# Kernel tuning notes

Measured on AMD Instinct MI355X. Metric: run time of the kernel, lower is better.

## Reference

```python
import jax, jax.numpy as jnp
import numpy as np

B, T, D, HD, HN, O = 32, 512, 512, 64, 16, 512
EPS = 1e-5


def setup_inputs() -> dict:
    key = jax.random.key(0)
    ks = jax.random.split(key, 12)
    s = lambda fan_in: 1.0 / np.sqrt(fan_in)
    inp = {
        "inputs": jax.random.normal(ks[0], (B, T, D), dtype=jnp.float32),
        "Wq": jax.random.uniform(ks[1], (HN, D, HD), jnp.float32, -s(D), s(D)),
        "bq": jnp.zeros((HN, HD), jnp.float32),
        "Wk": jax.random.uniform(ks[2], (HN, D, HD), jnp.float32, -s(D), s(D)),
        "bk": jnp.zeros((HN, HD), jnp.float32),
        "Wv": jax.random.uniform(ks[3], (HN, D, HD), jnp.float32, -s(D), s(D)),
        "bv": jnp.zeros((HN, HD), jnp.float32),
        "Wr": jax.random.uniform(ks[4], (D, O), jnp.float32, -s(D), s(D)),
        "br": jnp.zeros((O,), jnp.float32),
        "Wo": jax.random.uniform(ks[5], (HN * HD, O), jnp.float32, -s(HN * HD), s(HN * HD)),
        "bo": jnp.zeros((O,), jnp.float32),
        "ln1_w": jnp.ones((O,), jnp.float32),
        "ln1_b": jnp.zeros((O,), jnp.float32),
        "Wfc": jax.random.uniform(ks[6], (O, O), jnp.float32, -s(O), s(O)),
        "bfc": jnp.zeros((O,), jnp.float32),
        "ln2_w": jnp.ones((O,), jnp.float32),
        "ln2_b": jnp.zeros((O,), jnp.float32),
    }
    return inp


def _layernorm(x, w, b):
    mu = jnp.mean(x, axis=-1, keepdims=True)
    var = jnp.mean(jnp.square(x - mu), axis=-1, keepdims=True)
    return (x - mu) * jax.lax.rsqrt(var + EPS) * w + b


def reference(inputs, Wq, bq, Wk, bk, Wv, bv, Wr, br, Wo, bo,
              ln1_w, ln1_b, Wfc, bfc, ln2_w, ln2_b):
    # causal mask: multiply-then-subtract as in the original
    score_mask = jnp.tril(jnp.ones((T, T), jnp.float32))        # [T,T]
    padding_mask = (score_mask == 0).astype(jnp.float32) * 1e9  # [T,T]

    residual = inputs @ Wr + br                                  # [B,T,O]

    # batched per-head projections with nonstandard activations
    q = jax.nn.relu(jnp.einsum('btd,hdf->bhtf', inputs, Wq) + bq[None, :, None, :])
    k = jax.nn.relu(jnp.einsum('btd,hdf->bhtf', inputs, Wk) + bk[None, :, None, :])
    v = jnp.tanh(jnp.einsum('btd,hdf->bhtf', inputs, Wv) + bv[None, :, None, :])

    scores = jnp.einsum('bhtf,bhsf->bhts', q, k) / jnp.sqrt(jnp.float32(HD))
    scores = scores * score_mask - padding_mask                  # [B,H,T,T]
    weights = jax.nn.softmax(scores, axis=-1)
    heads = jnp.einsum('bhts,bhsf->bhtf', weights, v)            # [B,H,T,HD]

    # concat heads (head order preserved) + tanh output projection
    concat = heads.transpose(0, 2, 1, 3).reshape(B, T, HN * HD)
    out = jnp.tanh(concat @ Wo + bo)                             # [B,T,O]

    out = _layernorm(out + residual, ln1_w, ln1_b)
    fc = jax.nn.relu(out @ Wfc + bfc)
    out = _layernorm(fc + out, ln2_w, ln2_b)
    return out
```

## Files before the change

kernel.cpp:

```cpp
#include <hip/hip_runtime.h>
#include <hip/hip_bf16.h>

#define B_  32
#define T_  512
#define D_  512
#define HD_ 64
#define HN_ 16
#define O_  512
#define M_  (B_ * T_)
#define NQ_ (HN_ * HD_)

typedef __bf16 bf16;
typedef __attribute__((ext_vector_type(8))) __bf16 bf16x8;
typedef __attribute__((ext_vector_type(4))) __bf16 bf16x4;
typedef __attribute__((ext_vector_type(4))) float f32x4;

static __device__ __forceinline__ f32x4 mfma16(bf16x8 a, bf16x8 b, f32x4 c) {
    return __builtin_amdgcn_mfma_f32_16x16x32_bf16(a, b, c, 0, 0, 0);
}

static __device__ __forceinline__ void load_lds_16B(const bf16* g, bf16* l) {
    __builtin_amdgcn_global_load_lds(
        (const __attribute__((address_space(1))) unsigned int*)(unsigned long long)g,
        (__attribute__((address_space(3))) unsigned int*)(unsigned long long)l,
        16, 0, 0);
}

static __device__ __forceinline__ float fast_tanh(float x) {
    return 1.f - 2.f / (__expf(2.f * x) + 1.f);
}

static __device__ __forceinline__ int2 swz_block() {
    const int nx = gridDim.x;
    const int nwg = nx * gridDim.y;
    int l = blockIdx.y * nx + blockIdx.x;
    l = (l & 7) * (nwg >> 3) + (l >> 3);
    return make_int2(l % nx, l / nx);
}

__global__ __launch_bounds__(256) void prep_headw_kernel(
    const float* __restrict__ Wq, const float* __restrict__ Wk,
    const float* __restrict__ Wv, bf16* __restrict__ wall)
{
    __shared__ bf16 tl[64][72];
    int id = blockIdx.x;
    const int kt = id & 7; id >>= 3;
    const int h = id & 15; id >>= 4;
    const float* src = (id == 0) ? Wq : (id == 1) ? Wk : Wv;
    bf16* dst = wall + (size_t)id * (1024 * 512);
    const int tid = threadIdx.x;
    const int k0 = kt * 64;
#pragma unroll
    for (int i = 0; i < 4; i++) {
        const int e = i * 256 + tid;
        const int kk = e >> 4, f4 = (e & 15) * 4;
        const f32x4 v = *(const f32x4*)(src + ((size_t)h * 512 + k0 + kk) * 64 + f4);
#pragma unroll
        for (int j = 0; j < 4; j++) tl[f4 + j][kk] = (bf16)v[j];
    }
    __syncthreads();
#pragma unroll
    for (int i = 0; i < 2; i++) {
        const int e = i * 256 + tid;
        const int f = e >> 3, kc = (e & 7) * 8;
        *(bf16x8*)(dst + ((size_t)h * 64 + f) * 512 + k0 + kc) = *(const bf16x8*)&tl[f][kc];
    }
}

__global__ __launch_bounds__(256) void prep_plain_kernel(
    const float* __restrict__ Wr, const float* __restrict__ Wo,
    const float* __restrict__ Wfc,
    bf16* __restrict__ wrt, bf16* __restrict__ wot, bf16* __restrict__ wfct)
{
    __shared__ bf16 tl[64][72];
    int id = blockIdx.x;
    const float* src; bf16* dst; int K;
    if (id < 64)       { src = Wr;  dst = wrt;  K = 512;  }
    else if (id < 192) { src = Wo;  dst = wot;  K = 1024; id -= 64; }
    else               { src = Wfc; dst = wfct; K = 512;  id -= 192; }
    const int kt = id >> 3, nt = id & 7;
    const int k0 = kt * 64, n0 = nt * 64;
    const int tid = threadIdx.x;
#pragma unroll
    for (int i = 0; i < 4; i++) {
        const int e = i * 256 + tid;
        const int kk = e >> 4, n4 = (e & 15) * 4;
        const f32x4 v = *(const f32x4*)(src + (size_t)(k0 + kk) * 512 + n0 + n4);
#pragma unroll
        for (int j = 0; j < 4; j++) tl[n4 + j][kk] = (bf16)v[j];
    }
    __syncthreads();
#pragma unroll
    for (int i = 0; i < 2; i++) {
        const int e = i * 256 + tid;
        const int nn = e >> 3, kc = (e & 7) * 8;
        *(bf16x8*)(dst + (size_t)(n0 + nn) * K + k0 + kc) = *(const bf16x8*)&tl[nn][kc];
    }
}

__global__ __launch_bounds__(256) void conv_input_kernel(
    const float* __restrict__ in, bf16* __restrict__ out)
{
    const size_t i = ((size_t)blockIdx.x * 256 + threadIdx.x) * 8;
    f32x4 x0 = *(const f32x4*)(in + i);
    f32x4 x1 = *(const f32x4*)(in + i + 4);
    bf16x8 v;
    v[0] = (bf16)x0[0]; v[1] = (bf16)x0[1]; v[2] = (bf16)x0[2]; v[3] = (bf16)x0[3];
    v[4] = (bf16)x1[0]; v[5] = (bf16)x1[1]; v[6] = (bf16)x1[2]; v[7] = (bf16)x1[3];
    *(bf16x8*)(out + i) = v;
}

__global__ __launch_bounds__(256) void pack_bias_kernel(
    const float* __restrict__ bq, const float* __restrict__ bk,
    const float* __restrict__ bv, const float* __restrict__ br,
    float* __restrict__ ball)
{
    const int i = blockIdx.x * 256 + threadIdx.x;
    float v = (i < 1024) ? bq[i]
            : (i < 2048) ? bk[i - 1024]
            : (i < 3072) ? bv[i - 2048] : br[i - 3072];
    ball[i] = v;
}

__device__ __forceinline__ void gemm_mainloop_p4(
    const bf16* __restrict__ A, const bf16* __restrict__ Wt,
    const int K, const int m0, const int n0, const int tid,
    bf16* SL, f32x4 (&acc)[4][4])
{
    const int lane = tid & 63;
    const int w = tid >> 6;
    const int wr = w >> 1, wc = w & 1;
    const int lr = lane & 15, lg = lane >> 4;
    const int nt = K >> 5;

    const int p0 = tid, p1 = tid + 256;
    const bf16* aS0 = A + (size_t)(m0 + (p0 >> 2)) * K + (p0 & 3) * 8;
    const bf16* aS1 = A + (size_t)(m0 + (p1 >> 2)) * K + (p1 & 3) * 8;
    const bf16* bS0 = Wt + (size_t)(n0 + (p0 >> 2)) * K + (p0 & 3) * 8;
    const bf16* bS1 = Wt + (size_t)(n0 + (p1 >> 2)) * K + (p1 & 3) * 8;

    auto STAGE = [&](int t) {
        bf16* Ab = SL + (t & 3) * 4096;
        bf16* Bb = SL + 16384 + (t & 3) * 4096;
        const int k0 = t << 5;
        load_lds_16B(aS0 + k0, Ab + p0 * 8);
        load_lds_16B(aS1 + k0, Ab + p1 * 8);
        load_lds_16B(bS0 + k0, Bb + p0 * 8);
        load_lds_16B(bS1 + k0, Bb + p1 * 8);
    };

    STAGE(0); STAGE(1);
    asm volatile("s_waitcnt vmcnt(4)" ::: "memory");
    __builtin_amdgcn_s_barrier();

    for (int t = 0; t < nt; t++) {
        if (t + 2 < nt) {
            STAGE(t + 2);
            asm volatile("s_waitcnt vmcnt(4)" ::: "memory");
        } else {
            asm volatile("s_waitcnt vmcnt(0)" ::: "memory");
        }
        __builtin_amdgcn_s_barrier();
        const bf16* Ab = SL + (t & 3) * 4096;
        const bf16* Bb = SL + 16384 + (t & 3) * 4096;
        bf16x8 a[4], b[4];
#pragma unroll
        for (int mi = 0; mi < 4; mi++)
            a[mi] = *(const bf16x8*)&Ab[(wr * 64 + mi * 16 + lr) * 32 + lg * 8];
#pragma unroll
        for (int nj = 0; nj < 4; nj++)
            b[nj] = *(const bf16x8*)&Bb[(wc * 64 + nj * 16 + lr) * 32 + lg * 8];
        __builtin_amdgcn_s_setprio(1);
#pragma unroll
        for (int mi = 0; mi < 4; mi++)
#pragma unroll
            for (int nj = 0; nj < 4; nj++)
                acc[mi][nj] = mfma16(a[mi], b[nj], acc[mi][nj]);
        __builtin_amdgcn_s_setprio(0);
    }
    __builtin_amdgcn_s_barrier();
}

template <int ACT>
__device__ __forceinline__ void epi_transpose_store(
    f32x4 (&acc)[4][4], const float* __restrict__ ball, bf16* SL,
    bf16* __restrict__ dst, const int pitch, const int m0, const int nglob0,
    const int nb, const float scale, const int tid)
{
    const int lane = tid & 63, w = tid >> 6;
    const int wr = w >> 1, wc = w & 1, lr = lane & 15, lg = lane >> 4;
#pragma unroll
    for (int mi = 0; mi < 4; mi++) {
#pragma unroll
        for (int nj = 0; nj < 4; nj++) {
            const float bn = ball[nglob0 + wc * 64 + nj * 16 + lr];
            const int rbase = wr * 64 + mi * 16 + lg * 4;
            const int cidx = wc * 64 + nj * 16 + lr;
#pragma unroll
            for (int r = 0; r < 4; r++) {
                float v = acc[mi][nj][r] + bn;
                if constexpr (ACT == 1) v = fmaxf(v, 0.f);
                SL[(rbase + r) * 136 + cidx] = (bf16)(v * scale);
            }
        }
    }
    __syncthreads();
#pragma unroll
    for (int pass = 0; pass < 4; pass++) {
        const int rr = pass * 32 + (tid >> 3);
        const int cc = (tid & 7) * 16;
        bf16x8 v0 = *(const bf16x8*)&SL[rr * 136 + cc];
        bf16x8 v1 = *(const bf16x8*)&SL[rr * 136 + cc + 8];
        *(bf16x8*)(dst + (size_t)(m0 + rr) * pitch + nb + cc) = v0;
        *(bf16x8*)(dst + (size_t)(m0 + rr) * pitch + nb + cc + 8) = v1;
    }
}

__global__ __launch_bounds__(256) void gemm_qkvr_kernel(
    const bf16* __restrict__ A, const bf16* __restrict__ Wall,
    const float* __restrict__ ball,
    bf16* __restrict__ qc, bf16* __restrict__ kb, bf16* __restrict__ vt,
    bf16* __restrict__ resb)
{
    __shared__ bf16 SL[32768];
    const int tid = threadIdx.x;
    const int2 bc = swz_block();
    const int m0 = bc.y * 128, n0 = bc.x * 128;
    f32x4 acc[4][4];
    const f32x4 zero4 = {0.f, 0.f, 0.f, 0.f};
#pragma unroll
    for (int i = 0; i < 4; i++)
#pragma unroll
        for (int j = 0; j < 4; j++) acc[i][j] = zero4;

    gemm_mainloop_p4(A, Wall, 512, m0, n0, tid, SL, acc);

    const int region = n0 >> 10;
    if (region == 0) {
        epi_transpose_store<1>(acc, ball, SL, qc, 1024, m0, n0, n0 & 1023, 0.125f, tid);
    } else if (region == 1) {
        epi_transpose_store<1>(acc, ball, SL, kb, 1024, m0, n0, n0 & 1023, 1.f, tid);
    } else if (region == 3) {
        epi_transpose_store<0>(acc, ball, SL, resb, 512, m0, n0, n0 - 3072, 1.f, tid);
    } else {
        const int lane = tid & 63, w = tid >> 6;
        const int wr = w >> 1, wc = w & 1, lr = lane & 15, lg = lane >> 4;
#pragma unroll
        for (int mi = 0; mi < 4; mi++) {
#pragma unroll
            for (int nj = 0; nj < 4; nj++) {
                const int n = n0 + wc * 64 + nj * 16 + lr;
                const float bn = ball[n];
                const int m = m0 + wr * 64 + mi * 16 + lg * 4;
                const int bb = m >> 9, t = m & 511;
                const int nn = n - 2048, hh = nn >> 6, f = nn & 63;
                bf16x4 st;
#pragma unroll
                for (int r = 0; r < 4; r++) st[r] = (bf16)fast_tanh(acc[mi][nj][r] + bn);
                *(bf16x4*)(vt + (((size_t)(bb * 16 + hh) * 64 + f) << 9) + t) = st;
            }
        }
    }
}

template <int ACT>
__global__ __launch_bounds__(256) void gemm_std_kernel(
    const bf16* __restrict__ A, const bf16* __restrict__ Wt,
    const float* __restrict__ bias, bf16* __restrict__ C, const int K)
{
    __shared__ bf16 SL[32768];
    const int tid = threadIdx.x;
    const int2 bc = swz_block();
    const int m0 = bc.y * 128, n0 = bc.x * 128;
    f32x4 acc[4][4];
    const f32x4 zero4 = {0.f, 0.f, 0.f, 0.f};
#pragma unroll
    for (int i = 0; i < 4; i++)
#pragma unroll
        for (int j = 0; j < 4; j++) acc[i][j] = zero4;

    gemm_mainloop_p4(A, Wt, K, m0, n0, tid, SL, acc);

    const int lane = tid & 63, w = tid >> 6;
    const int wr = w >> 1, wc = w & 1, lr = lane & 15, lg = lane >> 4;
#pragma unroll
    for (int mi = 0; mi < 4; mi++) {
#pragma unroll
        for (int nj = 0; nj < 4; nj++) {
            const float bn = bias[n0 + wc * 64 + nj * 16 + lr];
            const int rbase = wr * 64 + mi * 16 + lg * 4;
            const int cidx = wc * 64 + nj * 16 + lr;
#pragma unroll
            for (int r = 0; r < 4; r++) {
                float v = acc[mi][nj][r] + bn;
                if constexpr (ACT == 1) v = fmaxf(v, 0.f);
                else if constexpr (ACT == 2) v = fast_tanh(v);
                SL[(rbase + r) * 136 + cidx] = (bf16)v;
            }
        }
    }
    __syncthreads();
#pragma unroll
    for (int pass = 0; pass < 4; pass++) {
        const int rr = pass * 32 + (tid >> 3);
        const int cc = (tid & 7) * 16;
        bf16x8 v0 = *(const bf16x8*)&SL[rr * 136 + cc];
        bf16x8 v1 = *(const bf16x8*)&SL[rr * 136 + cc + 8];
        *(bf16x8*)(C + (size_t)(m0 + rr) * 512 + n0 + cc) = v0;
        *(bf16x8*)(C + (size_t)(m0 + rr) * 512 + n0 + cc + 8) = v1;
    }
}

static __device__ __forceinline__ int sigma_k(int t) {
    return (t & 32) | ((t & 4) << 2) | ((t & 24) >> 1) | (t & 3);
}

__global__ __launch_bounds__(256) void mfma_attn_kernel(
    const bf16* __restrict__ Kb, const bf16* __restrict__ Vt, bf16* __restrict__ QC)
{
    __shared__ bf16 Ks[2][64][72];
    __shared__ bf16 Vts[2][64][72];

    int l = blockIdx.x;
    l = (l & 7) * 256 + (l >> 3);
    const int qb = l & 3;
    const int h = (l >> 2) & 15;
    const int b = l >> 6;
    const int tid = threadIdx.x;
    const int lane = tid & 63;
    const int w = tid >> 6;
    const int lr = lane & 15, lg = lane >> 4;

    const int qrow0 = qb * 128 + w * 32;
    const size_t qbase = ((size_t)b * T_ + qrow0) * NQ_ + h * 64;
    const int bh = b * HN_ + h;

    bf16x8 qf[2][2];
#pragma unroll
    for (int mi = 0; mi < 2; mi++)
#pragma unroll
        for (int kc = 0; kc < 2; kc++)
            qf[mi][kc] = *(const bf16x8*)(QC + qbase + (size_t)(mi * 16 + lr) * NQ_ + kc * 32 + lg * 8);

    const f32x4 zero4 = {0.f, 0.f, 0.f, 0.f};
    f32x4 o[2][4];
    float m_st[2] = {-1e30f, -1e30f}, l_st[2] = {0.f, 0.f};
#pragma unroll
    for (int mi = 0; mi < 2; mi++)
#pragma unroll
        for (int dj = 0; dj < 4; dj++) o[mi][dj] = zero4;

    const int nsb = 2 * qb + 2;

    bf16x8 kreg[2], vreg[2];
    auto LOADR = [&](int sb) {
#pragma unroll
        for (int i = 0; i < 2; i++) {
            const int ci = i * 256 + tid, row = ci >> 3, cc = ci & 7;
            kreg[i] = *(const bf16x8*)(Kb + ((size_t)b * T_ + sb * 64 + row) * NQ_ + h * 64 + cc * 8);
            vreg[i] = *(const bf16x8*)(Vt + ((size_t)bh * 64 + row) * T_ + sb * 64 + cc * 8);
        }
    };
    auto WRITE = [&](int buf) {
#pragma unroll
        for (int i = 0; i < 2; i++) {
            const int ci = i * 256 + tid, row = ci >> 3, cc = ci & 7;
            *(bf16x8*)&Ks[buf][sigma_k(row)][cc * 8] = kreg[i];
            *(bf16x8*)&Vts[buf][row][cc * 8] = vreg[i];
        }
    };

    LOADR(0); WRITE(0); __syncthreads();
    int cur = 0;

    for (int sb = 0; sb < nsb; sb++) {
        const bool pf = (sb + 1 < nsb);
        if (pf) LOADR(sb + 1);

        if (sb * 64 <= qrow0 + 31) {
            f32x4 sc[2][4];
#pragma unroll
            for (int mi = 0; mi < 2; mi++)
#pragma unroll
                for (int nj = 0; nj < 4; nj++) sc[mi][nj] = zero4;
            __builtin_amdgcn_s_setprio(1);
#pragma unroll
            for (int kc = 0; kc < 2; kc++) {
                bf16x8 kf[4];
#pragma unroll
                for (int nj = 0; nj < 4; nj++)
                    kf[nj] = *(const bf16x8*)&Ks[cur][nj * 16 + lr][kc * 32 + lg * 8];
#pragma unroll
                for (int mi = 0; mi < 2; mi++)
#pragma unroll
                    for (int nj = 0; nj < 4; nj++)
                        sc[mi][nj] = mfma16(kf[nj], qf[mi][kc], sc[mi][nj]);
            }
            __builtin_amdgcn_s_setprio(0);
            const bool needmask = (sb * 64 + 63 > qrow0);
            float tm[2];
#pragma unroll
            for (int mi = 0; mi < 2; mi++) {
                const int qg = qrow0 + mi * 16 + lr;
                float mx = -1e30f;
#pragma unroll
                for (int nj = 0; nj < 4; nj++) {
                    const int kvb = sb * 64 + ((nj >> 1) << 5) + ((nj & 1) << 2) + lg * 8;
#pragma unroll
                    for (int r = 0; r < 4; r++) {
                        float s = sc[mi][nj][r];
                        if (needmask && (kvb + r > qg)) s = -1e30f;
                        sc[mi][nj][r] = s;
                        mx = fmaxf(mx, s);
                    }
                }
                mx = fmaxf(mx, __shfl_xor(mx, 16));
                mx = fmaxf(mx, __shfl_xor(mx, 32));
                tm[mi] = mx;
            }
            const bool defer = (tm[0] <= m_st[0] + 8.f) && (tm[1] <= m_st[1] + 8.f);
            if (!__all(defer)) {
#pragma unroll
                for (int mi = 0; mi < 2; mi++) {
                    const float mn = fmaxf(m_st[mi], tm[mi]);
                    const float sf = __expf(m_st[mi] - mn);
                    m_st[mi] = mn;
                    l_st[mi] *= sf;
#pragma unroll
                    for (int dj = 0; dj < 4; dj++)
#pragma unroll
                        for (int r = 0; r < 4; r++) o[mi][dj][r] *= sf;
                }
            }
            bf16x4 pk[2][4];
#pragma unroll
            for (int mi = 0; mi < 2; mi++) {
                float ts = 0.f;
#pragma unroll
                for (int nj = 0; nj < 4; nj++)
#pragma unroll
                    for (int r = 0; r < 4; r++) {
                        const float p = __expf(sc[mi][nj][r] - m_st[mi]);
                        ts += p;
                        pk[mi][nj][r] = (bf16)p;
                    }
                ts += __shfl_xor(ts, 16);
                ts += __shfl_xor(ts, 32);
                l_st[mi] += ts;
            }
            __builtin_amdgcn_s_setprio(1);
#pragma unroll
            for (int kc = 0; kc < 2; kc++) {
                bf16x8 vf[4], pf2[2];
#pragma unroll
                for (int mi = 0; mi < 2; mi++) {
                    bf16x8 t;
#pragma unroll
                    for (int r = 0; r < 4; r++) { t[r] = pk[mi][2 * kc][r]; t[r + 4] = pk[mi][2 * kc + 1][r]; }
                    pf2[mi] = t;
                }
#pragma unroll
                for (int dj = 0; dj < 4; dj++)
                    vf[dj] = *(const bf16x8*)&Vts[cur][dj * 16 + lr][kc * 32 + lg * 8];
#pragma unroll
                for (int mi = 0; mi < 2; mi++)
#pragma unroll
                    for (int dj = 0; dj < 4; dj++)
                        o[mi][dj] = mfma16(vf[dj], pf2[mi], o[mi][dj]);
            }
            __builtin_amdgcn_s_setprio(0);
        }

        if (pf) WRITE(cur ^ 1);
        __syncthreads();
        cur ^= 1;
    }

#pragma unroll
    for (int mi = 0; mi < 2; mi++) {
        const float inv = 1.f / l_st[mi];
        const size_t rowoff = qbase + (size_t)(mi * 16 + lr) * NQ_;
#pragma unroll
        for (int dj = 0; dj < 4; dj++) {
            bf16x4 st;
#pragma unroll
            for (int r = 0; r < 4; r++) st[r] = (bf16)(o[mi][dj][r] * inv);
            *(bf16x4*)(QC + rowoff + dj * 16 + lg * 4) = st;
        }
    }
}

template <bool F32OUT>
__global__ __launch_bounds__(256) void ln_kernel(
    const bf16* __restrict__ xa, const bf16* __restrict__ xb,
    const float* __restrict__ w, const float* __restrict__ bias,
    void* __restrict__ outv)
{
    const int row = blockIdx.x * 4 + (threadIdx.x >> 6);
    const int ln = threadIdx.x & 63;
    const size_t base = (size_t)row * 512 + ln * 8;
    const bf16x8 va = *(const bf16x8*)(xa + base);
    const bf16x8 vb = *(const bf16x8*)(xb + base);
    float x[8];
    float s = 0.f;
#pragma unroll
    for (int i = 0; i < 8; i++) { x[i] = (float)va[i] + (float)vb[i]; s += x[i]; }
#pragma unroll
    for (int off = 32; off >= 1; off >>= 1) s += __shfl_xor(s, off);
    const float mean = s * (1.f / 512.f);
    float ss = 0.f;
#pragma unroll
    for (int i = 0; i < 8; i++) { x[i] -= mean; ss += x[i] * x[i]; }
#pragma unroll
    for (int off = 32; off >= 1; off >>= 1) ss += __shfl_xor(ss, off);
    const float inv = rsqrtf(ss * (1.f / 512.f) + 1e-5f);
    const f32x4 w0 = *(const f32x4*)(w + ln * 8);
    const f32x4 w1 = *(const f32x4*)(w + ln * 8 + 4);
    const f32x4 b0 = *(const f32x4*)(bias + ln * 8);
    const f32x4 b1 = *(const f32x4*)(bias + ln * 8 + 4);
    if constexpr (F32OUT) {
        f32x4 y0, y1;
#pragma unroll
        for (int i = 0; i < 4; i++) {
            y0[i] = x[i] * inv * w0[i] + b0[i];
            y1[i] = x[4 + i] * inv * w1[i] + b1[i];
        }
        *(f32x4*)((float*)outv + base) = y0;
        *(f32x4*)((float*)outv + base + 4) = y1;
    } else {
        bf16x8 y;
#pragma unroll
        for (int i = 0; i < 4; i++) {
            y[i] = (bf16)(x[i] * inv * w0[i] + b0[i]);
            y[4 + i] = (bf16)(x[4 + i] * inv * w1[i] + b1[i]);
        }
        *(bf16x8*)((bf16*)outv + base) = y;
    }
}

extern "C" void kernel_launch(void* const* d_in, const int* in_sizes, int n_in,
                              void* d_out, int out_size, void* d_ws, size_t ws_size,
                              hipStream_t stream)
{
    const float* inputs = (const float*)d_in[0];
    const float* Wq = (const float*)d_in[1];
    const float* bq = (const float*)d_in[2];
    const float* Wk = (const float*)d_in[3];
    const float* bk = (const float*)d_in[4];
    const float* Wv = (const float*)d_in[5];
    const float* bv = (const float*)d_in[6];
    const float* Wr = (const float*)d_in[7];
    const float* br = (const float*)d_in[8];
    const float* Wo = (const float*)d_in[9];
    const float* bo = (const float*)d_in[10];
    const float* ln1w = (const float*)d_in[11];
    const float* ln1b = (const float*)d_in[12];
    const float* Wfc = (const float*)d_in[13];
    const float* bfc = (const float*)d_in[14];
    const float* ln2w = (const float*)d_in[15];
    const float* ln2b = (const float*)d_in[16];
    float* out = (float*)d_out;

    const size_t MB = 1024ull * 1024ull;
    char* ws = (char*)d_ws;
    bf16* qc   = (bf16*)(ws);
    bf16* kb   = (bf16*)(ws + 32 * MB);
    bf16* vt   = (bf16*)(ws + 64 * MB);
    bf16* xin  = (bf16*)(ws + 96 * MB);
    bf16* wall = (bf16*)(ws + 112 * MB);
    bf16* wot  = (bf16*)(ws + 112 * MB + 3670016);
    bf16* wfct = (bf16*)(ws + 112 * MB + 3670016 + 1048576);
    float* ball = (float*)(ws + 112 * MB + 3670016 + 1048576 + 524288);
    bf16* wrt  = wall + (size_t)3072 * 512;
    bf16* resb = (bf16*)d_out;
    bf16* att  = kb;
    bf16* ln1  = kb + (size_t)8 * MB;
    bf16* fcb  = vt;

    const dim3 blk(256);

    conv_input_kernel<<<dim3(4096), blk, 0, stream>>>(inputs, xin);
    prep_headw_kernel<<<dim3(384), blk, 0, stream>>>(Wq, Wk, Wv, wall);
    prep_plain_kernel<<<dim3(256), blk, 0, stream>>>(Wr, Wo, Wfc, wrt, wot, wfct);
    pack_bias_kernel<<<dim3(14), blk, 0, stream>>>(bq, bk, bv, br, ball);

    gemm_qkvr_kernel<<<dim3(28, 128), blk, 0, stream>>>(xin, wall, ball, qc, kb, vt, resb);
    mfma_attn_kernel<<<dim3(B_ * HN_ * 4), blk, 0, stream>>>(kb, vt, qc);
    gemm_std_kernel<2><<<dim3(4, 128), blk, 0, stream>>>(qc, wot, bo, att, 1024);
    ln_kernel<false><<<dim3(4096), blk, 0, stream>>>(att, resb, ln1w, ln1b, ln1);
    gemm_std_kernel<1><<<dim3(4, 128), blk, 0, stream>>>(ln1, wfct, bfc, fcb, 512);
    ln_kernel<true ><<<dim3(4096), blk, 0, stream>>>(fcb, ln1, ln2w, ln2b, out);
}
```

Measured before the change: 252.6 us.

## Double GEMM K-tile to 64 with XOR-swizzled LDS layout

```diff
diff --git a/kernel.cpp b/kernel.cpp
--- a/kernel.cpp
+++ b/kernel.cpp
@@ -122,7 +122,7 @@
     ball[i] = v;
 }
 
-__device__ __forceinline__ void gemm_mainloop_p4(
+__device__ __forceinline__ void gemm_mainloop_4x64(
     const bf16* __restrict__ A, const bf16* __restrict__ Wt,
     const int K, const int m0, const int n0, const int tid,
     bf16* SL, f32x4 (&acc)[4][4])
@@ -131,52 +131,60 @@
     const int w = tid >> 6;
     const int wr = w >> 1, wc = w & 1;
     const int lr = lane & 15, lg = lane >> 4;
-    const int nt = K >> 5;
-
-    const int p0 = tid, p1 = tid + 256;
-    const bf16* aS0 = A + (size_t)(m0 + (p0 >> 2)) * K + (p0 & 3) * 8;
-    const bf16* aS1 = A + (size_t)(m0 + (p1 >> 2)) * K + (p1 & 3) * 8;
-    const bf16* bS0 = Wt + (size_t)(n0 + (p0 >> 2)) * K + (p0 & 3) * 8;
-    const bf16* bS1 = Wt + (size_t)(n0 + (p1 >> 2)) * K + (p1 & 3) * 8;
+    const int nt = K >> 6;
 
     auto STAGE = [&](int t) {
-        bf16* Ab = SL + (t & 3) * 4096;
-        bf16* Bb = SL + 16384 + (t & 3) * 4096;
-        const int k0 = t << 5;
-        load_lds_16B(aS0 + k0, Ab + p0 * 8);
-        load_lds_16B(aS1 + k0, Ab + p1 * 8);
-        load_lds_16B(bS0 + k0, Bb + p0 * 8);
-        load_lds_16B(bS1 + k0, Bb + p1 * 8);
+        bf16* Ab = SL + (t & 3) * 8192;
+        bf16* Bb = SL + 32768 + (t & 3) * 8192;
+        const int k0 = t << 6;
+#pragma unroll
+        for (int i = 0; i < 4; i++) {
+            const int p = i * 256 + tid;
+            const int row = p >> 3;
+            const int g = (p & 7) ^ (row & 7);
+            load_lds_16B(A + (size_t)(m0 + row) * K + k0 + g * 8, Ab + p * 8);
+            load_lds_16B(Wt + (size_t)(n0 + row) * K + k0 + g * 8, Bb + p * 8);
+        }
     };
 
     STAGE(0); STAGE(1);
-    asm volatile("s_waitcnt vmcnt(4)" ::: "memory");
+    asm volatile("s_waitcnt vmcnt(8)" ::: "memory");
     __builtin_amdgcn_s_barrier();
 
     for (int t = 0; t < nt; t++) {
         if (t + 2 < nt) {
             STAGE(t + 2);
-            asm volatile("s_waitcnt vmcnt(4)" ::: "memory");
+            asm volatile("s_waitcnt vmcnt(16)" ::: "memory");
+        } else if (t + 1 < nt) {
+            asm volatile("s_waitcnt vmcnt(8)" ::: "memory");
         } else {
             asm volatile("s_waitcnt vmcnt(0)" ::: "memory");
         }
         __builtin_amdgcn_s_barrier();
-        const bf16* Ab = SL + (t & 3) * 4096;
-        const bf16* Bb = SL + 16384 + (t & 3) * 4096;
-        bf16x8 a[4], b[4];
-#pragma unroll
-        for (int mi = 0; mi < 4; mi++)
-            a[mi] = *(const bf16x8*)&Ab[(wr * 64 + mi * 16 + lr) * 32 + lg * 8];
-#pragma unroll
-        for (int nj = 0; nj < 4; nj++)
-            b[nj] = *(const bf16x8*)&Bb[(wc * 64 + nj * 16 + lr) * 32 + lg * 8];
-        __builtin_amdgcn_s_setprio(1);
-#pragma unroll
-        for (int mi = 0; mi < 4; mi++)
-#pragma unroll
-            for (int nj = 0; nj < 4; nj++)
-                acc[mi][nj] = mfma16(a[mi], b[nj], acc[mi][nj]);
-        __builtin_amdgcn_s_setprio(0);
+
+        const bf16* Ab = SL + (t & 3) * 8192;
+        const bf16* Bb = SL + 32768 + (t & 3) * 8192;
+#pragma unroll
+        for (int kc = 0; kc < 2; kc++) {
+            bf16x8 a[4], b[4];
+#pragma unroll
+            for (int mi = 0; mi < 4; mi++) {
+                const int row = wr * 64 + mi * 16 + lr;
+                a[mi] = *(const bf16x8*)&Ab[row * 64 + ((((kc << 2) | lg) ^ (row & 7)) << 3)];
+            }
+#pragma unroll
+            for (int nj = 0; nj < 4; nj++) {
+                const int row = wc * 64 + nj * 16 + lr;
+                b[nj] = *(const bf16x8*)&Bb[row * 64 + ((((kc << 2) | lg) ^ (row & 7)) << 3)];
+            }
+            __builtin_amdgcn_s_setprio(1);
+#pragma unroll
+            for (int mi = 0; mi < 4; mi++)
+#pragma unroll
+                for (int nj = 0; nj < 4; nj++)
+                    acc[mi][nj] = mfma16(a[mi], b[nj], acc[mi][nj]);
+            __builtin_amdgcn_s_setprio(0);
+        }
     }
     __builtin_amdgcn_s_barrier();
 }
@@ -216,13 +224,13 @@
     }
 }
 
-__global__ __launch_bounds__(256) void gemm_qkvr_kernel(
+__global__ __launch_bounds__(256, 1) void gemm_qkvr_kernel(
     const bf16* __restrict__ A, const bf16* __restrict__ Wall,
     const float* __restrict__ ball,
     bf16* __restrict__ qc, bf16* __restrict__ kb, bf16* __restrict__ vt,
     bf16* __restrict__ resb)
 {
-    __shared__ bf16 SL[32768];
+    __shared__ bf16 SL[65536];
     const int tid = threadIdx.x;
     const int2 bc = swz_block();
     const int m0 = bc.y * 128, n0 = bc.x * 128;
@@ -233,7 +241,7 @@
 #pragma unroll
         for (int j = 0; j < 4; j++) acc[i][j] = zero4;
 
-    gemm_mainloop_p4(A, Wall, 512, m0, n0, tid, SL, acc);
+    gemm_mainloop_4x64(A, Wall, 512, m0, n0, tid, SL, acc);
 
     const int region = n0 >> 10;
     if (region == 0) {
@@ -264,11 +272,11 @@
 }
 
 template <int ACT>
-__global__ __launch_bounds__(256) void gemm_std_kernel(
+__global__ __launch_bounds__(256, 1) void gemm_std_kernel(
     const bf16* __restrict__ A, const bf16* __restrict__ Wt,
     const float* __restrict__ bias, bf16* __restrict__ C, const int K)
 {
-    __shared__ bf16 SL[32768];
+    __shared__ bf16 SL[65536];
     const int tid = threadIdx.x;
     const int2 bc = swz_block();
     const int m0 = bc.y * 128, n0 = bc.x * 128;
@@ -279,7 +287,7 @@
 #pragma unroll
         for (int j = 0; j < 4; j++) acc[i][j] = zero4;
 
-    gemm_mainloop_p4(A, Wt, K, m0, n0, tid, SL, acc);
+    gemm_mainloop_4x64(A, Wt, K, m0, n0, tid, SL, acc);
 
     const int lane = tid & 63, w = tid >> 6;
     const int wr = w >> 1, wc = w & 1, lr = lane & 15, lg = lane >> 4;
```

Result: slower. 269.1 us (+6.5%).

## Fuse prep kernels into one launch and XOR-swizzle GEMM LDS tiles

Applied to the files above, without the earlier changes.

```diff
diff --git a/kernel.cpp b/kernel.cpp
--- a/kernel.cpp
+++ b/kernel.cpp
@@ -38,84 +38,81 @@
     return make_int2(l % nx, l / nx);
 }
 
-__global__ __launch_bounds__(256) void prep_headw_kernel(
+__global__ __launch_bounds__(256) void prep_all_kernel(
+    const float* __restrict__ inputs,
     const float* __restrict__ Wq, const float* __restrict__ Wk,
-    const float* __restrict__ Wv, bf16* __restrict__ wall)
-{
-    __shared__ bf16 tl[64][72];
-    int id = blockIdx.x;
-    const int kt = id & 7; id >>= 3;
-    const int h = id & 15; id >>= 4;
-    const float* src = (id == 0) ? Wq : (id == 1) ? Wk : Wv;
-    bf16* dst = wall + (size_t)id * (1024 * 512);
-    const int tid = threadIdx.x;
-    const int k0 = kt * 64;
-#pragma unroll
-    for (int i = 0; i < 4; i++) {
-        const int e = i * 256 + tid;
-        const int kk = e >> 4, f4 = (e & 15) * 4;
-        const f32x4 v = *(const f32x4*)(src + ((size_t)h * 512 + k0 + kk) * 64 + f4);
-#pragma unroll
-        for (int j = 0; j < 4; j++) tl[f4 + j][kk] = (bf16)v[j];
-    }
-    __syncthreads();
-#pragma unroll
-    for (int i = 0; i < 2; i++) {
-        const int e = i * 256 + tid;
-        const int f = e >> 3, kc = (e & 7) * 8;
-        *(bf16x8*)(dst + ((size_t)h * 64 + f) * 512 + k0 + kc) = *(const bf16x8*)&tl[f][kc];
-    }
-}
-
-__global__ __launch_bounds__(256) void prep_plain_kernel(
-    const float* __restrict__ Wr, const float* __restrict__ Wo,
-    const float* __restrict__ Wfc,
-    bf16* __restrict__ wrt, bf16* __restrict__ wot, bf16* __restrict__ wfct)
-{
-    __shared__ bf16 tl[64][72];
-    int id = blockIdx.x;
-    const float* src; bf16* dst; int K;
-    if (id < 64)       { src = Wr;  dst = wrt;  K = 512;  }
-    else if (id < 192) { src = Wo;  dst = wot;  K = 1024; id -= 64; }
-    else               { src = Wfc; dst = wfct; K = 512;  id -= 192; }
-    const int kt = id >> 3, nt = id & 7;
-    const int k0 = kt * 64, n0 = nt * 64;
-    const int tid = threadIdx.x;
-#pragma unroll
-    for (int i = 0; i < 4; i++) {
-        const int e = i * 256 + tid;
-        const int kk = e >> 4, n4 = (e & 15) * 4;
-        const f32x4 v = *(const f32x4*)(src + (size_t)(k0 + kk) * 512 + n0 + n4);
-#pragma unroll
-        for (int j = 0; j < 4; j++) tl[n4 + j][kk] = (bf16)v[j];
-    }
-    __syncthreads();
-#pragma unroll
-    for (int i = 0; i < 2; i++) {
-        const int e = i * 256 + tid;
-        const int nn = e >> 3, kc = (e & 7) * 8;
-        *(bf16x8*)(dst + (size_t)(n0 + nn) * K + k0 + kc) = *(const bf16x8*)&tl[nn][kc];
-    }
-}
-
-__global__ __launch_bounds__(256) void conv_input_kernel(
-    const float* __restrict__ in, bf16* __restrict__ out)
-{
-    const size_t i = ((size_t)blockIdx.x * 256 + threadIdx.x) * 8;
-    f32x4 x0 = *(const f32x4*)(in + i);
-    f32x4 x1 = *(const f32x4*)(in + i + 4);
-    bf16x8 v;
-    v[0] = (bf16)x0[0]; v[1] = (bf16)x0[1]; v[2] = (bf16)x0[2]; v[3] = (bf16)x0[3];
-    v[4] = (bf16)x1[0]; v[5] = (bf16)x1[1]; v[6] = (bf16)x1[2]; v[7] = (bf16)x1[3];
-    *(bf16x8*)(out + i) = v;
-}
-
-__global__ __launch_bounds__(256) void pack_bias_kernel(
+    const float* __restrict__ Wv, const float* __restrict__ Wr,
+    const float* __restrict__ Wo, const float* __restrict__ Wfc,
     const float* __restrict__ bq, const float* __restrict__ bk,
     const float* __restrict__ bv, const float* __restrict__ br,
+    bf16* __restrict__ xin, bf16* __restrict__ wall,
+    bf16* __restrict__ wrt, bf16* __restrict__ wot, bf16* __restrict__ wfct,
     float* __restrict__ ball)
 {
-    const int i = blockIdx.x * 256 + threadIdx.x;
+    __shared__ bf16 tl[64][72];
+    const int tid = threadIdx.x;
+    int id = blockIdx.x;
+
+    if (id < 4096) {
+        const size_t i = ((size_t)id * 256 + tid) * 8;
+        f32x4 x0 = *(const f32x4*)(inputs + i);
+        f32x4 x1 = *(const f32x4*)(inputs + i + 4);
+        bf16x8 v;
+        v[0] = (bf16)x0[0]; v[1] = (bf16)x0[1]; v[2] = (bf16)x0[2]; v[3] = (bf16)x0[3];
+        v[4] = (bf16)x1[0]; v[5] = (bf16)x1[1]; v[6] = (bf16)x1[2]; v[7] = (bf16)x1[3];
+        *(bf16x8*)(xin + i) = v;
+        return;
+    }
+    if (id < 4480) {
+        id -= 4096;
+        const int kt = id & 7; id >>= 3;
+        const int h = id & 15; id >>= 4;
+        const float* src = (id == 0) ? Wq : (id == 1) ? Wk : Wv;
+        bf16* dst = wall + (size_t)id * (1024 * 512);
+        const int k0 = kt * 64;
+#pragma unroll
+        for (int i = 0; i < 4; i++) {
+            const int e = i * 256 + tid;
+            const int kk = e >> 4, f4 = (e & 15) * 4;
+            const f32x4 v = *(const f32x4*)(src + ((size_t)h * 512 + k0 + kk) * 64 + f4);
+#pragma unroll
+            for (int j = 0; j < 4; j++) tl[f4 + j][kk] = (bf16)v[j];
+        }
+        __syncthreads();
+#pragma unroll
+        for (int i = 0; i < 2; i++) {
+            const int e = i * 256 + tid;
+            const int f = e >> 3, kc = (e & 7) * 8;
+            *(bf16x8*)(dst + ((size_t)h * 64 + f) * 512 + k0 + kc) = *(const bf16x8*)&tl[f][kc];
+        }
+        return;
+    }
+    if (id < 4736) {
+        id -= 4480;
+        const float* src; bf16* dst; int K;
+        if (id < 64)       { src = Wr;  dst = wrt;  K = 512;  }
+        else if (id < 192) { src = Wo;  dst = wot;  K = 1024; id -= 64; }
+        else               { src = Wfc; dst = wfct; K = 512;  id -= 192; }
+        const int kt = id >> 3, nt = id & 7;
+        const int k0 = kt * 64, n0 = nt * 64;
+#pragma unroll
+        for (int i = 0; i < 4; i++) {
+            const int e = i * 256 + tid;
+            const int kk = e >> 4, n4 = (e & 15) * 4;
+            const f32x4 v = *(const f32x4*)(src + (size_t)(k0 + kk) * 512 + n0 + n4);
+#pragma unroll
+            for (int j = 0; j < 4; j++) tl[n4 + j][kk] = (bf16)v[j];
+        }
+        __syncthreads();
+#pragma unroll
+        for (int i = 0; i < 2; i++) {
+            const int e = i * 256 + tid;
+            const int nn = e >> 3, kc = (e & 7) * 8;
+            *(bf16x8*)(dst + (size_t)(n0 + nn) * K + k0 + kc) = *(const bf16x8*)&tl[nn][kc];
+        }
+        return;
+    }
+    const int i = (id - 4736) * 256 + tid;
     float v = (i < 1024) ? bq[i]
             : (i < 2048) ? bk[i - 1024]
             : (i < 3072) ? bv[i - 2048] : br[i - 3072];
@@ -133,20 +130,23 @@
     const int lr = lane & 15, lg = lane >> 4;
     const int nt = K >> 5;
 
-    const int p0 = tid, p1 = tid + 256;
-    const bf16* aS0 = A + (size_t)(m0 + (p0 >> 2)) * K + (p0 & 3) * 8;
-    const bf16* aS1 = A + (size_t)(m0 + (p1 >> 2)) * K + (p1 & 3) * 8;
-    const bf16* bS0 = Wt + (size_t)(n0 + (p0 >> 2)) * K + (p0 & 3) * 8;
-    const bf16* bS1 = Wt + (size_t)(n0 + (p1 >> 2)) * K + (p1 & 3) * 8;
+    const int r0 = tid >> 2, s0 = tid & 3;
+    const int g0 = s0 ^ ((r0 >> 1) & 3);
+    const int r1 = r0 + 64;
+    const int g1 = s0 ^ ((r1 >> 1) & 3);
+    const bf16* aS0 = A + (size_t)(m0 + r0) * K + g0 * 8;
+    const bf16* aS1 = A + (size_t)(m0 + r1) * K + g1 * 8;
+    const bf16* bS0 = Wt + (size_t)(n0 + r0) * K + g0 * 8;
+    const bf16* bS1 = Wt + (size_t)(n0 + r1) * K + g1 * 8;
 
     auto STAGE = [&](int t) {
         bf16* Ab = SL + (t & 3) * 4096;
         bf16* Bb = SL + 16384 + (t & 3) * 4096;
         const int k0 = t << 5;
-        load_lds_16B(aS0 + k0, Ab + p0 * 8);
-        load_lds_16B(aS1 + k0, Ab + p1 * 8);
-        load_lds_16B(bS0 + k0, Bb + p0 * 8);
-        load_lds_16B(bS1 + k0, Bb + p1 * 8);
+        load_lds_16B(aS0 + k0, Ab + tid * 8);
+        load_lds_16B(aS1 + k0, Ab + (tid + 256) * 8);
+        load_lds_16B(bS0 + k0, Bb + tid * 8);
+        load_lds_16B(bS1 + k0, Bb + (tid + 256) * 8);
     };
 
     STAGE(0); STAGE(1);
@@ -161,15 +161,20 @@
             asm volatile("s_waitcnt vmcnt(0)" ::: "memory");
         }
         __builtin_amdgcn_s_barrier();
+
         const bf16* Ab = SL + (t & 3) * 4096;
         const bf16* Bb = SL + 16384 + (t & 3) * 4096;
         bf16x8 a[4], b[4];
 #pragma unroll
-        for (int mi = 0; mi < 4; mi++)
-            a[mi] = *(const bf16x8*)&Ab[(wr * 64 + mi * 16 + lr) * 32 + lg * 8];
-#pragma unroll
-        for (int nj = 0; nj < 4; nj++)
-            b[nj] = *(const bf16x8*)&Bb[(wc * 64 + nj * 16 + lr) * 32 + lg * 8];
+        for (int mi = 0; mi < 4; mi++) {
+            const int row = wr * 64 + mi * 16 + lr;
+            a[mi] = *(const bf16x8*)&Ab[row * 32 + ((lg ^ ((row >> 1) & 3)) << 3)];
+        }
+#pragma unroll
+        for (int nj = 0; nj < 4; nj++) {
+            const int row = wc * 64 + nj * 16 + lr;
+            b[nj] = *(const bf16x8*)&Bb[row * 32 + ((lg ^ ((row >> 1) & 3)) << 3)];
+        }
         __builtin_amdgcn_s_setprio(1);
 #pragma unroll
         for (int mi = 0; mi < 4; mi++)
@@ -579,10 +584,9 @@
 
     const dim3 blk(256);
 
-    conv_input_kernel<<<dim3(4096), blk, 0, stream>>>(inputs, xin);
-    prep_headw_kernel<<<dim3(384), blk, 0, stream>>>(Wq, Wk, Wv, wall);
-    prep_plain_kernel<<<dim3(256), blk, 0, stream>>>(Wr, Wo, Wfc, wrt, wot, wfct);
-    pack_bias_kernel<<<dim3(14), blk, 0, stream>>>(bq, bk, bv, br, ball);
+    prep_all_kernel<<<dim3(4750), blk, 0, stream>>>(
+        inputs, Wq, Wk, Wv, Wr, Wo, Wfc, bq, bk, bv, br,
+        xin, wall, wrt, wot, wfct, ball);
 
     gemm_qkvr_kernel<<<dim3(28, 128), blk, 0, stream>>>(xin, wall, ball, qc, kb, vt, resb);
     mfma_attn_kernel<<<dim3(B_ * HN_ * 4), blk, 0, stream>>>(kb, vt, qc);
```

Result: faster. 241.5 us (-4.4%).
